# Optimization experiments

Hardware: AMD Instinct MI355X
Metric: run time of the kernel (lower is better)

Reference implementation:

```python
import math
import jax, jax.numpy as jnp
import numpy as np

B, V, F, H, W = 1, 2, 4, 16, 28
TPF = H * W            # 448 tokens per frame
VS = F * TPF           # 1792 tokens per view
TS = V * VS            # 3584 total tokens
DIM, NH = 1536, 12
HD = DIM // NH         # 128
EPS = 1e-6
SCALE = 1.0 / math.sqrt(HD)


def _rope_angle_table(max_len=1024):
    # Wan-style 3D rope: head_dim//2 = 64 channels split [22, 21, 21] for (f, h, w)
    parts = []
    for full in (44, 42, 42):
        inv = 1.0 / (10000.0 ** (np.arange(0, full, 2) / full))
        parts.append(np.outer(np.arange(max_len), inv))
    return np.concatenate(parts, axis=1).astype(np.float32)  # [max_len, 64]


def setup_inputs():
    key = jax.random.key(0)
    ks = jax.random.split(key, 6)
    p = lambda k, shp: 0.02 * jax.random.normal(k, shp, dtype=jnp.float32)
    return {
        "x": jax.random.normal(ks[0], (B, TS, DIM), dtype=jnp.float32),
        "freqs": jnp.asarray(_rope_angle_table()),
        "q_w": p(ks[1], (DIM, DIM)), "q_b": jnp.zeros((DIM,), jnp.float32),
        "k_w": p(ks[2], (DIM, DIM)), "k_b": jnp.zeros((DIM,), jnp.float32),
        "v_w": p(ks[3], (DIM, DIM)), "v_b": jnp.zeros((DIM,), jnp.float32),
        "o_w": p(ks[4], (DIM, DIM)), "o_b": jnp.zeros((DIM,), jnp.float32),
        "norm_q_w": jnp.ones((DIM,), jnp.float32),
        "norm_k_w": jnp.ones((DIM,), jnp.float32),
        "seq_lens": jnp.full((B,), TS, jnp.int32),
        "view_grid_sizes": jnp.broadcast_to(jnp.array([F, H, W], jnp.int32), (B, V, 3)),
        "view_seq_lens": jnp.full((B, V), VS, jnp.int32),
        "total_seq_lens": jnp.full((B,), TS, jnp.int32),
    }


def _rms_norm(x, w):
    x32 = x.astype(jnp.float32)
    y = x32 * jax.lax.rsqrt(jnp.mean(x32 * x32, axis=-1, keepdims=True) + EPS)
    return y.astype(x.dtype) * w


def _rope_angles(freqs):
    c = HD // 2                                   # 64
    s0, s1 = c - 2 * (c // 3), c // 3             # 22, 21
    af = jnp.broadcast_to(freqs[:F, None, None, :s0], (F, H, W, s0))
    ah = jnp.broadcast_to(freqs[None, :H, None, s0:s0 + s1], (F, H, W, s1))
    aw = jnp.broadcast_to(freqs[None, None, :W, s0 + s1:c], (F, H, W, c - s0 - s1))
    return jnp.concatenate([af, ah, aw], axis=-1).reshape(VS, c)  # [VS, 64]


def _apply_rope(x, ang):
    # x: [N, S, NH, HD]; pairs are (x[..., 2i], x[..., 2i+1]) as in view_as_complex
    cos = jnp.cos(ang)[None, :, None, :]
    sin = jnp.sin(ang)[None, :, None, :]
    xr = x.reshape(x.shape[:-1] + (HD // 2, 2))
    r0 = xr[..., 0] * cos - xr[..., 1] * sin
    r1 = xr[..., 0] * sin + xr[..., 1] * cos
    return jnp.stack([r0, r1], axis=-1).reshape(x.shape)


def _attn_lse(q, k, v):
    # q,k,v: [N, S, NH, HD] -> out [N, S, NH, HD], lse [N, S, NH]
    logits = jnp.einsum('bqhd,bkhd->bhqk', q, k) * SCALE
    lse = jax.nn.logsumexp(logits, axis=-1)       # [N, NH, Sq]
    p = jnp.exp(logits - lse[..., None])
    out = jnp.einsum('bhqk,bkhd->bqhd', p, v)
    return out, jnp.transpose(lse, (0, 2, 1))


def _forward(x, freqs, q_w, q_b, k_w, k_b, v_w, v_b, o_w, o_b, norm_q_w, norm_k_w):
    xv = x[:, :TS]
    q = _rms_norm(xv @ q_w.T + q_b, norm_q_w)
    k = _rms_norm(xv @ k_w.T + k_b, norm_k_w)
    v = xv @ v_w.T + v_b
    q = q.reshape(B * V, VS, NH, HD)
    k = k.reshape(B * V, VS, NH, HD)
    v = v.reshape(B * V, VS, NH, HD)
    ang = _rope_angles(freqs)
    q = _apply_rope(q, ang)
    k = _apply_rope(k, ang)
    # intra-view attention over the full view sequence
    out_i, lse_i = _attn_lse(q, k, v)
    # cross-view per-frame attention: swap the two views for K/V
    k_sw = k.reshape(B, V, F, TPF, NH, HD)[:, ::-1].reshape(B * V * F, TPF, NH, HD)
    v_sw = v.reshape(B, V, F, TPF, NH, HD)[:, ::-1].reshape(B * V * F, TPF, NH, HD)
    q_c = q.reshape(B * V * F, TPF, NH, HD)
    out_c, lse_c = _attn_lse(q_c, k_sw, v_sw)
    out_i = out_i.reshape(B, V, F, TPF, NH, HD)
    lse_i = lse_i.reshape(B, V, F, TPF, NH)
    out_c = out_c.reshape(B, V, F, TPF, NH, HD)
    lse_c = lse_c.reshape(B, V, F, TPF, NH)
    # online-softmax-style LSE merge of the two attention results
    lse_u = jnp.logaddexp(lse_i, lse_c)
    fused = (jnp.exp(lse_i - lse_u)[..., None] * out_i
             + jnp.exp(lse_c - lse_u)[..., None] * out_c)
    fused = fused.reshape(B, TS, DIM)
    return fused @ o_w.T + o_b


def reference(x, freqs, q_w, q_b, k_w, k_b, v_w, v_b, o_w, o_b, norm_q_w, norm_k_w,
              seq_lens, view_grid_sizes, view_seq_lens, total_seq_lens):
    del seq_lens, view_grid_sizes, view_seq_lens, total_seq_lens  # validated layout constants
    return _forward(x, freqs, q_w, q_b, k_w, k_b, v_w, v_b, o_w, o_b, norm_q_w, norm_k_w)
```

## Files before the change

kernel.cpp:

```cpp
#include <hip/hip_runtime.h>

#define TS 3584
#define VS 1792
#define TPF 448
#define NHEAD 12
#define HDIM 128
#define DMODEL 1536
#define QK_PRESCALE (0.08838834764831845f * 1.4426950408889634f)

typedef unsigned short u16;
typedef unsigned int u32;
typedef unsigned long long u64;
typedef __attribute__((ext_vector_type(8))) short bf16x8;
typedef __attribute__((ext_vector_type(4))) float f32x4;

__device__ __forceinline__ float u2f(u32 u) { union { u32 u; float f; } c; c.u = u; return c.f; }
__device__ __forceinline__ float blo(u32 u) { return u2f(u << 16); }
__device__ __forceinline__ float bhi(u32 u) { return u2f(u & 0xffff0000u); }
__device__ __forceinline__ u16 f2b(float f) {
  union { float f; u32 u; } c; c.f = f;
  return (u16)((c.u + 0x7fffu + ((c.u >> 16) & 1u)) >> 16);
}

__device__ __forceinline__ float exp2fast(float x) {
#if __has_builtin(__builtin_amdgcn_exp2f)
  return __builtin_amdgcn_exp2f(x);
#else
  float r; asm("v_exp_f32 %0, %1" : "=v"(r) : "v"(x)); return r;
#endif
}

__device__ __forceinline__ void gl16(const u16* g, u16* l) {
  __builtin_amdgcn_global_load_lds(
      (const __attribute__((address_space(1))) void*)g,
      (__attribute__((address_space(3))) void*)l, 16, 0, 0);
}

__global__ __launch_bounds__(256) void convert_bf16(
    const float* __restrict__ x, const float* __restrict__ qw,
    const float* __restrict__ kw, const float* __restrict__ vw,
    const float* __restrict__ ow, u16* __restrict__ xb,
    u16* __restrict__ wqkv, u16* __restrict__ owb) {
  const int z = blockIdx.y;
  const float* src;
  u16* dst;
  int n8;
  if (z == 0)      { src = x;  dst = xb;  n8 = TS * DMODEL / 8; }
  else if (z == 4) { src = ow; dst = owb; n8 = DMODEL * DMODEL / 8; }
  else {
    src = (z == 1) ? qw : (z == 2) ? kw : vw;
    dst = wqkv + (size_t)(z - 1) * DMODEL * DMODEL;
    n8 = DMODEL * DMODEL / 8;
  }
  const int idx = blockIdx.x * 256 + threadIdx.x;
  if (idx >= n8) return;
  const float4 a = ((const float4*)src)[2 * idx];
  const float4 b = ((const float4*)src)[2 * idx + 1];
  uint4 o;
  o.x = (u32)f2b(a.x) | ((u32)f2b(a.y) << 16);
  o.y = (u32)f2b(a.z) | ((u32)f2b(a.w) << 16);
  o.z = (u32)f2b(b.x) | ((u32)f2b(b.y) << 16);
  o.w = (u32)f2b(b.z) | ((u32)f2b(b.w) << 16);
  ((uint4*)dst)[idx] = o;
}

template <bool QKV>
__global__ __launch_bounds__(256) void gemm_mfma(
    const u16* __restrict__ A, const u16* __restrict__ W,
    const float* __restrict__ b0, const float* __restrict__ b1,
    const float* __restrict__ b2,
    u16* __restrict__ o0, u16* __restrict__ o1, u16* __restrict__ o2,
    float* __restrict__ of) {
  __shared__ __align__(16) u16 SH[128 * 128];
  u16* const Als = SH;
  u16* const Bls = SH + 128 * 64;
  const int t = threadIdx.x;
  const int wave = t >> 6, lane = t & 63, col = lane & 15, quad = lane >> 4;
  const int nwg = gridDim.x * gridDim.y;
  const int dlin = blockIdx.y * gridDim.x + blockIdx.x;
  const int wk = (dlin & 7) * (nwg >> 3) + (dlin >> 3);
  const int by = wk / gridDim.x, bx = wk - by * gridDim.x;
  const int m0 = by * 128, n0 = bx * 128;
  const int wm = (wave & 1) * 64, wn = (wave >> 1) * 64;

  const int srow = lane >> 3;
  const int sch = (lane & 7) ^ srow;
  const u16* pA[4];
  const u16* pB[4];
#pragma unroll
  for (int i = 0; i < 4; ++i) {
    const int r = i * 32 + wave * 8 + srow;
    pA[i] = A + (size_t)(m0 + r) * DMODEL + sch * 8;
    pB[i] = W + (size_t)(n0 + r) * DMODEL + sch * 8;
  }

  f32x4 acc[4][4];
#pragma unroll
  for (int i = 0; i < 4; ++i)
#pragma unroll
    for (int j = 0; j < 4; ++j) acc[i][j] = (f32x4){0.f, 0.f, 0.f, 0.f};

  for (int k0 = 0; k0 < DMODEL; k0 += 64) {
    __syncthreads();
#pragma unroll
    for (int i = 0; i < 4; ++i) {
      gl16(pA[i] + k0, &Als[i * 2048 + wave * 512]);
      gl16(pB[i] + k0, &Bls[i * 2048 + wave * 512]);
    }
    __syncthreads();
#pragma unroll
    for (int s = 0; s < 2; ++s) {
      bf16x8 af[4], bv[4];
#pragma unroll
      for (int i = 0; i < 4; ++i) {
        const int r = wm + i * 16 + col;
        af[i] = *(const bf16x8*)&Als[r * 64 + (((s * 4 + quad) ^ (r & 7)) * 8)];
      }
#pragma unroll
      for (int j = 0; j < 4; ++j) {
        const int r = wn + j * 16 + col;
        bv[j] = *(const bf16x8*)&Bls[r * 64 + (((s * 4 + quad) ^ (r & 7)) * 8)];
      }
#pragma unroll
      for (int i = 0; i < 4; ++i)
#pragma unroll
        for (int j = 0; j < 4; ++j)
          acc[i][j] = __builtin_amdgcn_mfma_f32_16x16x32_bf16(af[i], bv[j], acc[i][j], 0, 0, 0);
    }
  }

  if constexpr (QKV) {
    const int sec = n0 / DMODEL;
    if (sec == 2) {
      __syncthreads();
#pragma unroll
      for (int j = 0; j < 4; ++j) {
        const int hdl = wn + j * 16 + col;
        const float bias = b2[n0 - 2 * DMODEL + hdl];
#pragma unroll
        for (int i = 0; i < 4; ++i) {
          const int tokl = wm + i * 16 + quad * 4;
          u64 pk = (u64)f2b(acc[i][j][0] + bias) |
                   ((u64)f2b(acc[i][j][1] + bias) << 16) |
                   ((u64)f2b(acc[i][j][2] + bias) << 32) |
                   ((u64)f2b(acc[i][j][3] + bias) << 48);
          *(u64*)&SH[hdl * 128 + (((tokl >> 3) ^ (hdl & 15)) * 8) + (tokl & 7)] = pk;
        }
      }
      __syncthreads();
      const int hgl = (n0 - 2 * DMODEL) >> 7;
#pragma unroll
      for (int it = 0; it < 8; ++it) {
        const int idx = t + it * 256;
        const int row = idx >> 4, ch = idx & 15;
        uint4 w = *(const uint4*)&SH[row * 128 + ((ch ^ (row & 15)) * 8)];
        *(uint4*)(o2 + (size_t)(hgl * HDIM + row) * TS + m0 + ch * 8) = w;
      }
      return;
    }
    u16* dst = (sec == 0) ? o0 : o1;
    const float* bp = (sec == 0) ? b0 : b1;
#pragma unroll
    for (int j = 0; j < 4; ++j) {
      const int nn = n0 - sec * DMODEL + wn + j * 16 + col;
      const float bias = bp[nn];
#pragma unroll
      for (int i = 0; i < 4; ++i) {
        const int mb = m0 + wm + i * 16 + quad * 4;
#pragma unroll
        for (int r = 0; r < 4; ++r)
          dst[(size_t)(mb + r) * DMODEL + nn] = f2b(acc[i][j][r] + bias);
      }
    }
  } else {
#pragma unroll
    for (int j = 0; j < 4; ++j) {
      const int ng = n0 + wn + j * 16 + col;
      const float bias = b0[ng];
#pragma unroll
      for (int i = 0; i < 4; ++i) {
        const int mb = m0 + wm + i * 16 + quad * 4;
#pragma unroll
        for (int r = 0; r < 4; ++r)
          of[(size_t)(mb + r) * DMODEL + ng] = acc[i][j][r] + bias;
      }
    }
  }
}

__global__ __launch_bounds__(256) void rmsnorm_rope(
    u16* qbuf, u16* kbuf, const float* __restrict__ freqs,
    const float* __restrict__ nqw, const float* __restrict__ nkw) {
  const int tok = blockIdx.x;
  u32* row = (u32*)((blockIdx.y == 0 ? qbuf : kbuf) + (size_t)tok * DMODEL);
  const float* w = blockIdx.y == 0 ? nqw : nkw;
  const int t = threadIdx.x;
  const u32 u0 = row[t], u1 = row[t + 256], u2 = row[t + 512];
  float px[3] = { blo(u0), blo(u1), blo(u2) };
  float py[3] = { bhi(u0), bhi(u1), bhi(u2) };
  float ss = px[0] * px[0] + py[0] * py[0] + px[1] * px[1] + py[1] * py[1] +
             px[2] * px[2] + py[2] * py[2];
#pragma unroll
  for (int off = 32; off; off >>= 1) ss += __shfl_xor(ss, off);
  __shared__ float red[4];
  if ((t & 63) == 0) red[t >> 6] = ss;
  __syncthreads();
  float rstd = rsqrtf((red[0] + red[1] + red[2] + red[3]) * (1.0f / DMODEL) + 1e-6f);
  if (blockIdx.y == 0) rstd *= QK_PRESCALE;
  const int p = tok % VS;
  const int fi = p / TPF, rem = p % TPF, hi = rem / 28, wi = rem % 28;
#pragma unroll
  for (int jj = 0; jj < 3; ++jj) {
    const int pj = t + jj * 256;
    const int i = pj & 63;
    const int prow = (i < 22) ? fi : ((i < 43) ? hi : wi);
    const float ang = freqs[prow * 64 + i];
    float sn, cs;
    sincosf(ang, &sn, &cs);
    const float a = px[jj] * rstd * w[2 * pj], b = py[jj] * rstd * w[2 * pj + 1];
    row[pj] = (u32)f2b(a * cs - b * sn) | ((u32)f2b(a * sn + b * cs) << 16);
  }
}

__global__ __launch_bounds__(128) void attn_mfma(
    const u16* __restrict__ q, const u16* __restrict__ k,
    const u16* __restrict__ vt, u16* __restrict__ fused) {
  __shared__ __align__(16) u16 Kls[2 * 32 * 128];
  __shared__ __align__(16) u16 Vls[2 * 128 * 32];
  const int t = threadIdx.x;
  const int wave = t >> 6, lane = t & 63;
  const int col = lane & 15, quad = lane >> 4;
  const int d = blockIdx.y * 56 + blockIdx.x;
  const int wk = (d & 7) * 84 + (d >> 3);
  const int h = wk / 56;
  const int qb = wk - h * 56;
  const int q0 = qb * 64;
  const int vview = q0 / VS;
  const int fidx = (q0 % VS) / TPF;
  const int base0 = vview * VS;
  const int base1 = (1 - vview) * VS + fidx * TPF;
  const int jmpd = base1 - base0 - 1760;

  const u16* qrow = q + (size_t)(q0 + wave * 32 + col) * DMODEL + h * HDIM;
  bf16x8 qfA[4], qfB[4];
#pragma unroll
  for (int c = 0; c < 4; ++c) {
    qfA[c] = *(const bf16x8*)(qrow + ((c * 4 + quad) << 3));
    qfB[c] = *(const bf16x8*)(qrow + 16 * DMODEL + ((c * 4 + quad) << 3));
  }
  asm volatile("" ::: "memory");

  const u16* ksrc[4];
  const u16* vsrc[4];
#pragma unroll
  for (int j = 0; j < 4; ++j) {
    const int ci = (wave * 4 + j) * 64 + lane;
    const int key = ci >> 4, c = ci & 15;
    const int k4 = ((key >> 1) & 12) | (key & 3);
    ksrc[j] = k + (size_t)(base0 + key) * DMODEL + h * HDIM + ((c ^ k4) << 3);
    const int hd = ci >> 2, sl = ci & 3;
    vsrc[j] = vt + (size_t)(h * HDIM + hd) * TS + base0 + ((sl ^ (hd & 3)) << 3);
  }
  const int r0 = ((col & 12) << 1) | (col & 3);
  int koffu[4];
#pragma unroll
  for (int c = 0; c < 4; ++c) koffu[c] = r0 * 128 + (((c * 4 + quad) ^ col) << 3);
  const int voffu = col * 32 + ((quad ^ (col & 3)) << 3);

#pragma unroll
  for (int j = 0; j < 4; ++j) {
    gl16(ksrc[j], &Kls[(wave * 4 + j) * 512]);
    gl16(vsrc[j], &Vls[(wave * 4 + j) * 512]);
  }
  int ts = 1;
#pragma unroll
  for (int j = 0; j < 4; ++j) { ksrc[j] += 32 * DMODEL; vsrc[j] += 32; }

  f32x4 accA[8], accB[8];
#pragma unroll
  for (int c = 0; c < 8; ++c) {
    accA[c] = (f32x4){0.f, 0.f, 0.f, 0.f};
    accB[c] = (f32x4){0.f, 0.f, 0.f, 0.f};
  }
  float mA = -1e30f, lA = 0.f, mB = -1e30f, lB = 0.f;

#define AITER(CUR, LAST)                                                       \
  do {                                                                         \
    if (!(LAST)) {                                                             \
      _Pragma("unroll") for (int j = 0; j < 4; ++j) {                          \
        gl16(ksrc[j], &Kls[((CUR) ^ 1) * 4096 + (wave * 4 + j) * 512]);        \
        gl16(vsrc[j], &Vls[((CUR) ^ 1) * 4096 + (wave * 4 + j) * 512]);        \
      }                                                                        \
      const int dd = (ts == 55) ? jmpd : 32; ++ts;                             \
      _Pragma("unroll") for (int j = 0; j < 4; ++j) {                          \
        ksrc[j] += (ptrdiff_t)dd * DMODEL; vsrc[j] += dd;                      \
      }                                                                        \
    }                                                                          \
    asm volatile("s_waitcnt vmcnt(%0)" ::"i"((LAST) ? 0 : 8) : "memory");      \
    __builtin_amdgcn_s_barrier();                                              \
    asm volatile("" ::: "memory");                                             \
    f32x4 s0a = (f32x4){0.f, 0.f, 0.f, 0.f}, s1a = s0a, s0b = s0a, s1b = s0a;  \
    __builtin_amdgcn_s_setprio(1);                                             \
    _Pragma("unroll") for (int c = 0; c < 4; ++c) {                            \
      bf16x8 ka0 = *(const bf16x8*)&Kls[(CUR) * 4096 + koffu[c]];              \
      bf16x8 ka1 = *(const bf16x8*)&Kls[(CUR) * 4096 + koffu[c] + 512];        \
      s0a = __builtin_amdgcn_mfma_f32_16x16x32_bf16(ka0, qfA[c], s0a, 0, 0, 0);\
      s1a = __builtin_amdgcn_mfma_f32_16x16x32_bf16(ka1, qfA[c], s1a, 0, 0, 0);\
      s0b = __builtin_amdgcn_mfma_f32_16x16x32_bf16(ka0, qfB[c], s0b, 0, 0, 0);\
      s1b = __builtin_amdgcn_mfma_f32_16x16x32_bf16(ka1, qfB[c], s1b, 0, 0, 0);\
    }                                                                          \
    __builtin_amdgcn_s_setprio(0);                                             \
    float lmaxA = fmaxf(fmaxf(fmaxf(s0a[0], s0a[1]), fmaxf(s0a[2], s0a[3])),   \
                        fmaxf(fmaxf(s1a[0], s1a[1]), fmaxf(s1a[2], s1a[3])));  \
    float lmaxB = fmaxf(fmaxf(fmaxf(s0b[0], s0b[1]), fmaxf(s0b[2], s0b[3])),   \
                        fmaxf(fmaxf(s1b[0], s1b[1]), fmaxf(s1b[2], s1b[3])));  \
    lmaxA = fmaxf(lmaxA, __shfl_xor(lmaxA, 16));                               \
    lmaxA = fmaxf(lmaxA, __shfl_xor(lmaxA, 32));                               \
    lmaxB = fmaxf(lmaxB, __shfl_xor(lmaxB, 16));                               \
    lmaxB = fmaxf(lmaxB, __shfl_xor(lmaxB, 32));                               \
    if (__any(fmaxf(lmaxA - mA, lmaxB - mB) > 8.f)) {                          \
      const float mnA = fmaxf(mA, lmaxA), mnB = fmaxf(mB, lmaxB);              \
      const float aA = exp2fast(mA - mnA), aB = exp2fast(mB - mnB);            \
      _Pragma("unroll") for (int c = 0; c < 8; ++c) {                          \
        accA[c][0] *= aA; accA[c][1] *= aA; accA[c][2] *= aA; accA[c][3] *= aA;\
        accB[c][0] *= aB; accB[c][1] *= aB; accB[c][2] *= aB; accB[c][3] *= aB;\
      }                                                                        \
      lA *= aA; lB *= aB; mA = mnA; mB = mnB;                                  \
    }                                                                          \
    float psA = 0.f, psB = 0.f;                                                \
    _Pragma("unroll") for (int r = 0; r < 4; ++r) {                            \
      s0a[r] = exp2fast(s0a[r] - mA); s1a[r] = exp2fast(s1a[r] - mA);          \
      s0b[r] = exp2fast(s0b[r] - mB); s1b[r] = exp2fast(s1b[r] - mB);          \
      psA += s0a[r] + s1a[r]; psB += s0b[r] + s1b[r];                          \
    }                                                                          \
    union { u32 w[4]; bf16x8 v; } puA, puB;                                    \
    asm("v_cvt_pk_bf16_f32 %0, %1, %2" : "=v"(puA.w[0]) : "v"(s0a[0]), "v"(s0a[1])); \
    asm("v_cvt_pk_bf16_f32 %0, %1, %2" : "=v"(puA.w[1]) : "v"(s0a[2]), "v"(s0a[3])); \
    asm("v_cvt_pk_bf16_f32 %0, %1, %2" : "=v"(puA.w[2]) : "v"(s1a[0]), "v"(s1a[1])); \
    asm("v_cvt_pk_bf16_f32 %0, %1, %2" : "=v"(puA.w[3]) : "v"(s1a[2]), "v"(s1a[3])); \
    asm("v_cvt_pk_bf16_f32 %0, %1, %2" : "=v"(puB.w[0]) : "v"(s0b[0]), "v"(s0b[1])); \
    asm("v_cvt_pk_bf16_f32 %0, %1, %2" : "=v"(puB.w[1]) : "v"(s0b[2]), "v"(s0b[3])); \
    asm("v_cvt_pk_bf16_f32 %0, %1, %2" : "=v"(puB.w[2]) : "v"(s1b[0]), "v"(s1b[1])); \
    asm("v_cvt_pk_bf16_f32 %0, %1, %2" : "=v"(puB.w[3]) : "v"(s1b[2]), "v"(s1b[3])); \
    __builtin_amdgcn_s_setprio(1);                                             \
    _Pragma("unroll") for (int c = 0; c < 8; ++c) {                            \
      bf16x8 va = *(const bf16x8*)&Vls[(CUR) * 4096 + voffu + c * 512];        \
      accA[c] = __builtin_amdgcn_mfma_f32_16x16x32_bf16(va, puA.v, accA[c], 0, 0, 0); \
      accB[c] = __builtin_amdgcn_mfma_f32_16x16x32_bf16(va, puB.v, accB[c], 0, 0, 0); \
    }                                                                          \
    __builtin_amdgcn_s_setprio(0);                                             \
    if (!(LAST)) {                                                             \
      asm volatile("" ::: "memory");                                           \
      __builtin_amdgcn_s_barrier();                                            \
      asm volatile("" ::: "memory");                                           \
    }                                                                          \
    psA += __shfl_xor(psA, 16);                                                \
    psA += __shfl_xor(psA, 32);                                                \
    psB += __shfl_xor(psB, 16);                                                \
    psB += __shfl_xor(psB, 32);                                                \
    lA += psA; lB += psB;                                                      \
  } while (0)

  for (int tt = 0; tt < 34; ++tt) {
    AITER(0, false);
    AITER(1, false);
  }
  AITER(0, false);
  AITER(1, true);
#undef AITER

  const float invA = 1.0f / lA, invB = 1.0f / lB;
  u16* orowA = fused + (size_t)(q0 + wave * 32 + col) * DMODEL + h * HDIM;
  u16* orowB = orowA + 16 * DMODEL;
#pragma unroll
  for (int c = 0; c < 8; ++c) {
    uint2 oa, ob;
    oa.x = (u32)f2b(accA[c][0] * invA) | ((u32)f2b(accA[c][1] * invA) << 16);
    oa.y = (u32)f2b(accA[c][2] * invA) | ((u32)f2b(accA[c][3] * invA) << 16);
    ob.x = (u32)f2b(accB[c][0] * invB) | ((u32)f2b(accB[c][1] * invB) << 16);
    ob.y = (u32)f2b(accB[c][2] * invB) | ((u32)f2b(accB[c][3] * invB) << 16);
    *(uint2*)(orowA + c * 16 + quad * 4) = oa;
    *(uint2*)(orowB + c * 16 + quad * 4) = ob;
  }
}

extern "C" void kernel_launch(void* const* d_in, const int* in_sizes, int n_in,
                              void* d_out, int out_size, void* d_ws, size_t ws_size,
                              hipStream_t stream) {
  (void)in_sizes; (void)n_in; (void)out_size; (void)ws_size;
  const float* x   = (const float*)d_in[0];
  const float* fr  = (const float*)d_in[1];
  const float* qw  = (const float*)d_in[2];
  const float* qb  = (const float*)d_in[3];
  const float* kw  = (const float*)d_in[4];
  const float* kb  = (const float*)d_in[5];
  const float* vw  = (const float*)d_in[6];
  const float* vb  = (const float*)d_in[7];
  const float* ow  = (const float*)d_in[8];
  const float* ob  = (const float*)d_in[9];
  const float* nqw = (const float*)d_in[10];
  const float* nkw = (const float*)d_in[11];

  u16* qf   = (u16*)d_ws;
  u16* vf   = qf + (size_t)TS * DMODEL;
  u16* xb   = vf + (size_t)TS * DMODEL;
  u16* wqkv = xb + (size_t)TS * DMODEL;
  u16* owb  = wqkv + (size_t)3 * DMODEL * DMODEL;
  u16* kf   = (u16*)d_out;
  u16* vtb  = (u16*)d_out + (size_t)TS * DMODEL;

  convert_bf16<<<dim3(TS * DMODEL / 8 / 256, 5), dim3(256), 0, stream>>>(
      x, qw, kw, vw, ow, xb, wqkv, owb);
  gemm_mfma<true><<<dim3(3 * DMODEL / 128, TS / 128), dim3(256), 0, stream>>>(
      xb, wqkv, qb, kb, vb, qf, kf, vtb, nullptr);
  rmsnorm_rope<<<dim3(TS, 2), dim3(256), 0, stream>>>(qf, kf, fr, nqw, nkw);
  attn_mfma<<<dim3(TS / 64, NHEAD), dim3(128), 0, stream>>>(qf, kf, vtb, qf);
  gemm_mfma<false><<<dim3(DMODEL / 128, TS / 128), dim3(256), 0, stream>>>(
      qf, owb, ob, nullptr, nullptr, nullptr, nullptr, nullptr, (float*)d_out);
}
```

Baseline: 332.6 us.

## Split attention KV range across two wave pairs and merge via LDS

The attention kernel now launches 256 threads per block. Two wave pairs each process half of the 70 key/value tiles for the same 64 query rows, and each pair has its own double-buffered K/V LDS region. At the end, the second pair writes its accumulators and softmax stats to LDS, and the first pair merges them with an LSE-style rescale before writing the output. This halves the serial KV loop per wave to raise parallelism and latency hiding. The cost is doubled LDS use per block, an extra merge pass through shared memory, and possibly lower occupancy.

```diff
diff --git a/kernel.cpp b/kernel.cpp
--- a/kernel.cpp
+++ b/kernel.cpp
@@ -222,14 +222,16 @@
   }
 }
 
-__global__ __launch_bounds__(128) void attn_mfma(
+__global__ __launch_bounds__(256) void attn_mfma(
     const u16* __restrict__ q, const u16* __restrict__ k,
     const u16* __restrict__ vt, u16* __restrict__ fused) {
-  __shared__ __align__(16) u16 Kls[2 * 32 * 128];
-  __shared__ __align__(16) u16 Vls[2 * 128 * 32];
+  __shared__ __align__(16) u16 Kls[2 * 2 * 4096];
+  __shared__ __align__(16) u16 Vls[2 * 2 * 4096];
   const int t = threadIdx.x;
   const int wave = t >> 6, lane = t & 63;
   const int col = lane & 15, quad = lane >> 4;
+  const int pair = wave >> 1;
+  const int pw = wave & 1;
   const int d = blockIdx.y * 56 + blockIdx.x;
   const int wk = (d & 7) * 84 + (d >> 3);
   const int h = wk / 56;
@@ -241,7 +243,7 @@
   const int base1 = (1 - vview) * VS + fidx * TPF;
   const int jmpd = base1 - base0 - 1760;
 
-  const u16* qrow = q + (size_t)(q0 + wave * 32 + col) * DMODEL + h * HDIM;
+  const u16* qrow = q + (size_t)(q0 + pw * 32 + col) * DMODEL + h * HDIM;
   bf16x8 qfA[4], qfB[4];
 #pragma unroll
   for (int c = 0; c < 4; ++c) {
@@ -250,29 +252,33 @@
   }
   asm volatile("" ::: "memory");
 
+  const int pstart = pair * 35;
   const u16* ksrc[4];
   const u16* vsrc[4];
 #pragma unroll
   for (int j = 0; j < 4; ++j) {
-    const int ci = (wave * 4 + j) * 64 + lane;
+    const int ci = (pw * 4 + j) * 64 + lane;
     const int key = ci >> 4, c = ci & 15;
     const int k4 = ((key >> 1) & 12) | (key & 3);
-    ksrc[j] = k + (size_t)(base0 + key) * DMODEL + h * HDIM + ((c ^ k4) << 3);
+    ksrc[j] = k + (size_t)(base0 + pstart * 32 + key) * DMODEL + h * HDIM +
+              ((c ^ k4) << 3);
     const int hd = ci >> 2, sl = ci & 3;
-    vsrc[j] = vt + (size_t)(h * HDIM + hd) * TS + base0 + ((sl ^ (hd & 3)) << 3);
+    vsrc[j] = vt + (size_t)(h * HDIM + hd) * TS + base0 + pstart * 32 +
+              ((sl ^ (hd & 3)) << 3);
   }
   const int r0 = ((col & 12) << 1) | (col & 3);
   int koffu[4];
 #pragma unroll
-  for (int c = 0; c < 4; ++c) koffu[c] = r0 * 128 + (((c * 4 + quad) ^ col) << 3);
-  const int voffu = col * 32 + ((quad ^ (col & 3)) << 3);
+  for (int c = 0; c < 4; ++c)
+    koffu[c] = pair * 8192 + r0 * 128 + (((c * 4 + quad) ^ col) << 3);
+  const int voffu = pair * 8192 + col * 32 + ((quad ^ (col & 3)) << 3);
 
 #pragma unroll
   for (int j = 0; j < 4; ++j) {
-    gl16(ksrc[j], &Kls[(wave * 4 + j) * 512]);
-    gl16(vsrc[j], &Vls[(wave * 4 + j) * 512]);
-  }
-  int ts = 1;
+    gl16(ksrc[j], &Kls[pair * 8192 + (pw * 4 + j) * 512]);
+    gl16(vsrc[j], &Vls[pair * 8192 + (pw * 4 + j) * 512]);
+  }
+  int ts = pstart + 1;
 #pragma unroll
   for (int j = 0; j < 4; ++j) { ksrc[j] += 32 * DMODEL; vsrc[j] += 32; }
 
@@ -288,8 +294,8 @@
   do {                                                                         \
     if (!(LAST)) {                                                             \
       _Pragma("unroll") for (int j = 0; j < 4; ++j) {                          \
-        gl16(ksrc[j], &Kls[((CUR) ^ 1) * 4096 + (wave * 4 + j) * 512]);        \
-        gl16(vsrc[j], &Vls[((CUR) ^ 1) * 4096 + (wave * 4 + j) * 512]);        \
+        gl16(ksrc[j], &Kls[pair * 8192 + ((CUR) ^ 1) * 4096 + (pw * 4 + j) * 512]); \
+        gl16(vsrc[j], &Vls[pair * 8192 + ((CUR) ^ 1) * 4096 + (pw * 4 + j) * 512]); \
       }                                                                        \
       const int dd = (ts == 55) ? jmpd : 32; ++ts;                             \
       _Pragma("unroll") for (int j = 0; j < 4; ++j) {                          \
@@ -361,26 +367,60 @@
     lA += psA; lB += psB;                                                      \
   } while (0)
 
-  for (int tt = 0; tt < 34; ++tt) {
+  for (int tt = 0; tt < 17; ++tt) {
     AITER(0, false);
     AITER(1, false);
   }
-  AITER(0, false);
-  AITER(1, true);
+  AITER(0, true);
 #undef AITER
 
-  const float invA = 1.0f / lA, invB = 1.0f / lB;
-  u16* orowA = fused + (size_t)(q0 + wave * 32 + col) * DMODEL + h * HDIM;
-  u16* orowB = orowA + 16 * DMODEL;
-#pragma unroll
-  for (int c = 0; c < 8; ++c) {
-    uint2 oa, ob;
-    oa.x = (u32)f2b(accA[c][0] * invA) | ((u32)f2b(accA[c][1] * invA) << 16);
-    oa.y = (u32)f2b(accA[c][2] * invA) | ((u32)f2b(accA[c][3] * invA) << 16);
-    ob.x = (u32)f2b(accB[c][0] * invB) | ((u32)f2b(accB[c][1] * invB) << 16);
-    ob.y = (u32)f2b(accB[c][2] * invB) | ((u32)f2b(accB[c][3] * invB) << 16);
-    *(uint2*)(orowA + c * 16 + quad * 4) = oa;
-    *(uint2*)(orowB + c * 16 + quad * 4) = ob;
+  __syncthreads();
+  float* M = (float*)Kls;
+  float* S = (float*)Vls;
+  if (wave >= 2) {
+    const int rg = pw * 4096;
+#pragma unroll
+    for (int c = 0; c < 8; ++c)
+#pragma unroll
+      for (int r = 0; r < 4; ++r) {
+        M[rg + (c * 4 + r) * 64 + lane] = accA[c][r];
+        M[rg + 2048 + (c * 4 + r) * 64 + lane] = accB[c][r];
+      }
+    S[pw * 256 + lane] = mA;
+    S[pw * 256 + 64 + lane] = lA;
+    S[pw * 256 + 128 + lane] = mB;
+    S[pw * 256 + 192 + lane] = lB;
+  }
+  __syncthreads();
+  if (wave < 2) {
+    const int rg = pw * 4096;
+    const float mAp = S[pw * 256 + lane];
+    const float lAp = S[pw * 256 + 64 + lane];
+    const float mBp = S[pw * 256 + 128 + lane];
+    const float lBp = S[pw * 256 + 192 + lane];
+    const float muA = fmaxf(mA, mAp), muB = fmaxf(mB, mBp);
+    const float sA = exp2fast(mA - muA), xA = exp2fast(mAp - muA);
+    const float sB = exp2fast(mB - muB), xB = exp2fast(mBp - muB);
+    const float invA = 1.0f / (lA * sA + lAp * xA);
+    const float invB = 1.0f / (lB * sB + lBp * xB);
+    u16* orowA = fused + (size_t)(q0 + pw * 32 + col) * DMODEL + h * HDIM;
+    u16* orowB = orowA + 16 * DMODEL;
+#pragma unroll
+    for (int c = 0; c < 8; ++c) {
+      float fa[4], fb[4];
+#pragma unroll
+      for (int r = 0; r < 4; ++r) {
+        fa[r] = (accA[c][r] * sA + M[rg + (c * 4 + r) * 64 + lane] * xA) * invA;
+        fb[r] = (accB[c][r] * sB + M[rg + 2048 + (c * 4 + r) * 64 + lane] * xB) * invB;
+      }
+      uint2 oa, ob;
+      oa.x = (u32)f2b(fa[0]) | ((u32)f2b(fa[1]) << 16);
+      oa.y = (u32)f2b(fa[2]) | ((u32)f2b(fa[3]) << 16);
+      ob.x = (u32)f2b(fb[0]) | ((u32)f2b(fb[1]) << 16);
+      ob.y = (u32)f2b(fb[2]) | ((u32)f2b(fb[3]) << 16);
+      *(uint2*)(orowA + c * 16 + quad * 4) = oa;
+      *(uint2*)(orowB + c * 16 + quad * 4) = ob;
+    }
   }
 }
 
@@ -414,7 +454,7 @@
   gemm_mfma<true><<<dim3(3 * DMODEL / 128, TS / 128), dim3(256), 0, stream>>>(
       xb, wqkv, qb, kb, vb, qf, kf, vtb, nullptr);
   rmsnorm_rope<<<dim3(TS, 2), dim3(256), 0, stream>>>(qf, kf, fr, nqw, nkw);
-  attn_mfma<<<dim3(TS / 64, NHEAD), dim3(128), 0, stream>>>(qf, kf, vtb, qf);
+  attn_mfma<<<dim3(TS / 64, NHEAD), dim3(256), 0, stream>>>(qf, kf, vtb, qf);
   gemm_mfma<false><<<dim3(DMODEL / 128, TS / 128), dim3(256), 0, stream>>>(
       qf, owb, ob, nullptr, nullptr, nullptr, nullptr, nullptr, (float*)d_out);
 }
```

Result: slower. 387.4 us (+16.5%).
